# Kernel tuning notes

Measured on AMD Instinct MI355X. Metric: run time of the kernel, lower is better.

Reference implementation:

```python
import jax, jax.numpy as jnp
import numpy as np

IN_FEATURES = 4096
OUT_FEATURES = 8192
LUT_SIZE = 65536  # 256 * 256 two-level codebook


def setup_inputs() -> dict:
    key = jax.random.key(0)
    k_x, k_b, k_f, k_s, k_l = jax.random.split(key, 5)
    x = jax.random.normal(k_x, (2, 256, IN_FEATURES), dtype=jnp.float32)
    base_idx = jax.random.randint(k_b, (OUT_FEATURES, IN_FEATURES), 0, 256, dtype=jnp.int32)
    fine_idx = jax.random.randint(k_f, (OUT_FEATURES, IN_FEATURES), 0, 256, dtype=jnp.int32)
    scale = jax.random.uniform(k_s, (OUT_FEATURES, 1), dtype=jnp.float32)
    lut = jax.random.normal(k_l, (LUT_SIZE,), dtype=jnp.float32)
    return {"x": x, "base_idx": base_idx, "fine_idx": fine_idx, "scale": scale, "lut": lut}


def reference(x, base_idx, fine_idx, scale, lut):
    # Two-level LUT dequant: combined 16-bit index = base*256 + fine
    combined_idx = base_idx * 256 + fine_idx              # [out, in] int32
    weights = lut[combined_idx] * scale                   # [out, in] fp32, per-row scale
    # F.linear(x, weights) == x @ weights.T
    return jnp.einsum('bsi,oi->bso', x, weights)
```

## Files before the change

kernel.cpp:

```cpp
#include <hip/hip_runtime.h>

typedef unsigned short ushort_t;
typedef unsigned int   uint32;
typedef __attribute__((ext_vector_type(8))) short short8;
typedef __attribute__((ext_vector_type(4))) float floatx4;

#define IN_F   4096
#define OUT_F  8192
#define M_TOT  512
#define NB     32
#define BK     64
#define WS     72
#define NITER  (IN_F / BK)

__device__ __forceinline__ ushort_t f2bf(float f) {
    uint32 u = __builtin_bit_cast(uint32, f);
    u += 0x7FFFu + ((u >> 16) & 1u);
    return (ushort_t)(u >> 16);
}

__global__ void cvt_x_kernel(const float* __restrict__ x, ushort_t* __restrict__ xb) {
    int i = (blockIdx.x * 256 + threadIdx.x) * 8;
    float4 v0 = *(const float4*)(x + i);
    float4 v1 = *(const float4*)(x + i + 4);
    short8 s;
    s[0] = (short)f2bf(v0.x); s[1] = (short)f2bf(v0.y);
    s[2] = (short)f2bf(v0.z); s[3] = (short)f2bf(v0.w);
    s[4] = (short)f2bf(v1.x); s[5] = (short)f2bf(v1.y);
    s[6] = (short)f2bf(v1.z); s[7] = (short)f2bf(v1.w);
    *(short8*)(xb + i) = s;
}

template<bool XBF16>
__global__ __launch_bounds__(512)
void ghost_kernel(const float* __restrict__ xf, const ushort_t* __restrict__ xb,
                  const int* __restrict__ base_idx, const int* __restrict__ fine_idx,
                  const float* __restrict__ scale, const float* __restrict__ lut,
                  float* __restrict__ out)
{
    __shared__ ushort_t sh_lut[65536];
    __shared__ ushort_t sh_w[2][NB * WS];

    const int tid = threadIdx.x;
    const int n0  = blockIdx.x * NB;

    for (int i = tid * 4; i < 65536; i += 512 * 4) {
        float4 v = *(const float4*)(lut + i);
        sh_lut[i + 0] = f2bf(v.x);
        sh_lut[i + 1] = f2bf(v.y);
        sh_lut[i + 2] = f2bf(v.z);
        sh_lut[i + 3] = f2bf(v.w);
    }

    const int sn  = tid >> 4;
    const int skq = (tid & 15) * 4;
    const int* bp = base_idx + (size_t)(n0 + sn) * IN_F + skq;
    const int* fp = fine_idx + (size_t)(n0 + sn) * IN_F + skq;

    __syncthreads();

    int4 pb = *(const int4*)(bp);
    int4 pf = *(const int4*)(fp);
    {
        uint32 w0 = (uint32)sh_lut[(pb.x << 8) + pf.x] | ((uint32)sh_lut[(pb.y << 8) + pf.y] << 16);
        uint32 w1 = (uint32)sh_lut[(pb.z << 8) + pf.z] | ((uint32)sh_lut[(pb.w << 8) + pf.w] << 16);
        uint2 wv; wv.x = w0; wv.y = w1;
        *(uint2*)&sh_w[0][sn * WS + skq] = wv;
    }
    pb = *(const int4*)(bp + BK);
    pf = *(const int4*)(fp + BK);
    __syncthreads();

    const int lane = tid & 63;
    const int wave = tid >> 6;
    const int l16  = lane & 15;
    const int quad = lane >> 4;
    const int mrow = wave * 64 + l16;

    floatx4 acc[4][2];
    const floatx4 zero = {0.f, 0.f, 0.f, 0.f};
#pragma unroll
    for (int f = 0; f < 4; ++f) { acc[f][0] = zero; acc[f][1] = zero; }

    const ushort_t* xrow  = XBF16 ? (xb + (size_t)mrow * IN_F + quad * 8) : (const ushort_t*)nullptr;
    const float*    xrowf = XBF16 ? (const float*)nullptr : (xf + (size_t)mrow * IN_F + quad * 8);

    for (int t = 0; t < NITER; ++t) {
        const int k0 = t * BK;

        {
            uint32 w0 = (uint32)sh_lut[(pb.x << 8) + pf.x] | ((uint32)sh_lut[(pb.y << 8) + pf.y] << 16);
            uint32 w1 = (uint32)sh_lut[(pb.z << 8) + pf.z] | ((uint32)sh_lut[(pb.w << 8) + pf.w] << 16);
            uint2 wv; wv.x = w0; wv.y = w1;
            *(uint2*)&sh_w[(t + 1) & 1][sn * WS + skq] = wv;
        }
        {
            const int kk = (t + 2 < NITER ? t + 2 : NITER - 1) * BK;
            pb = *(const int4*)(bp + kk);
            pf = *(const int4*)(fp + kk);
        }

        const ushort_t* wb = sh_w[t & 1];
#pragma unroll
        for (int ks = 0; ks < 2; ++ks) {
            const int kk = k0 + ks * 32;
            short8 b0 = *(const short8*)&wb[l16        * WS + ks * 32 + quad * 8];
            short8 b1 = *(const short8*)&wb[(16 + l16) * WS + ks * 32 + quad * 8];
#pragma unroll
            for (int f = 0; f < 4; ++f) {
                short8 a;
                if (XBF16) {
                    a = *(const short8*)(xrow + (size_t)f * 16 * IN_F + kk);
                } else {
                    const float* p = xrowf + (size_t)f * 16 * IN_F + kk;
                    float4 u0 = *(const float4*)p;
                    float4 u1 = *(const float4*)(p + 4);
                    a[0] = (short)f2bf(u0.x); a[1] = (short)f2bf(u0.y);
                    a[2] = (short)f2bf(u0.z); a[3] = (short)f2bf(u0.w);
                    a[4] = (short)f2bf(u1.x); a[5] = (short)f2bf(u1.y);
                    a[6] = (short)f2bf(u1.z); a[7] = (short)f2bf(u1.w);
                }
                acc[f][0] = __builtin_amdgcn_mfma_f32_16x16x32_bf16(a, b0, acc[f][0], 0, 0, 0);
                acc[f][1] = __builtin_amdgcn_mfma_f32_16x16x32_bf16(a, b1, acc[f][1], 0, 0, 0);
            }
        }
        __syncthreads();
    }

#pragma unroll
    for (int nf = 0; nf < 2; ++nf) {
        const int col = n0 + nf * 16 + l16;
        const float sc = scale[col];
#pragma unroll
        for (int f = 0; f < 4; ++f) {
            const int r0 = wave * 64 + f * 16 + quad * 4;
#pragma unroll
            for (int r = 0; r < 4; ++r) {
                out[(size_t)(r0 + r) * OUT_F + col] = acc[f][nf][r] * sc;
            }
        }
    }
}

extern "C" void kernel_launch(void* const* d_in, const int* in_sizes, int n_in,
                              void* d_out, int out_size, void* d_ws, size_t ws_size,
                              hipStream_t stream) {
    const float* x      = (const float*)d_in[0];
    const int*   bidx   = (const int*)d_in[1];
    const int*   fidx   = (const int*)d_in[2];
    const float* scale  = (const float*)d_in[3];
    const float* lut    = (const float*)d_in[4];
    float*       out    = (float*)d_out;

    const size_t xb_bytes = (size_t)M_TOT * IN_F * sizeof(ushort_t);
    if (ws_size >= xb_bytes) {
        ushort_t* xb = (ushort_t*)d_ws;
        cvt_x_kernel<<<1024, 256, 0, stream>>>(x, xb);
        ghost_kernel<true><<<OUT_F / NB, 512, 0, stream>>>(x, xb, bidx, fidx, scale, lut, out);
    } else {
        ghost_kernel<false><<<OUT_F / NB, 512, 0, stream>>>(x, nullptr, bidx, fidx, scale, lut, out);
    }
}
```

Before: 392.8 us.

## Double block to 1024 threads with 16 waves and BK=128 weight tiles

Raises the thread block from 512 to 1024 threads (16 waves), each wave now covering 32 rows of M instead of 64, and doubles the K tile to 128 so each barrier-separated step does twice the MFMA work. The aim is more latency hiding from extra waves while the 128KB shared LUT still limits the CU to one block, plus fewer syncs per output tile. The trade-off is that each wave reuses its B fragments across fewer A rows, and the double-buffered weight tile uses more shared memory.

```diff
diff --git a/kernel.cpp b/kernel.cpp
--- a/kernel.cpp
+++ b/kernel.cpp
@@ -9,8 +9,8 @@
 #define OUT_F  8192
 #define M_TOT  512
 #define NB     32
-#define BK     64
-#define WS     72
+#define BK     128
+#define WS     136
 #define NITER  (IN_F / BK)
 
 __device__ __forceinline__ ushort_t f2bf(float f) {
@@ -32,7 +32,7 @@
 }
 
 template<bool XBF16>
-__global__ __launch_bounds__(512)
+__global__ __launch_bounds__(1024, 4)
 void ghost_kernel(const float* __restrict__ xf, const ushort_t* __restrict__ xb,
                   const int* __restrict__ base_idx, const int* __restrict__ fine_idx,
                   const float* __restrict__ scale, const float* __restrict__ lut,
@@ -44,7 +44,7 @@
     const int tid = threadIdx.x;
     const int n0  = blockIdx.x * NB;
 
-    for (int i = tid * 4; i < 65536; i += 512 * 4) {
+    for (int i = tid * 4; i < 65536; i += 1024 * 4) {
         float4 v = *(const float4*)(lut + i);
         sh_lut[i + 0] = f2bf(v.x);
         sh_lut[i + 1] = f2bf(v.y);
@@ -52,8 +52,8 @@
         sh_lut[i + 3] = f2bf(v.w);
     }
 
-    const int sn  = tid >> 4;
-    const int skq = (tid & 15) * 4;
+    const int sn  = tid >> 5;
+    const int skq = (tid & 31) * 4;
     const int* bp = base_idx + (size_t)(n0 + sn) * IN_F + skq;
     const int* fp = fine_idx + (size_t)(n0 + sn) * IN_F + skq;
 
@@ -75,13 +75,12 @@
     const int wave = tid >> 6;
     const int l16  = lane & 15;
     const int quad = lane >> 4;
-    const int mrow = wave * 64 + l16;
 
-    floatx4 acc[4][2];
+    floatx4 acc[2][2];
     const floatx4 zero = {0.f, 0.f, 0.f, 0.f};
-#pragma unroll
-    for (int f = 0; f < 4; ++f) { acc[f][0] = zero; acc[f][1] = zero; }
+    acc[0][0] = zero; acc[0][1] = zero; acc[1][0] = zero; acc[1][1] = zero;
 
+    const int mrow = wave * 32 + l16;
     const ushort_t* xrow  = XBF16 ? (xb + (size_t)mrow * IN_F + quad * 8) : (const ushort_t*)nullptr;
     const float*    xrowf = XBF16 ? (const float*)nullptr : (xf + (size_t)mrow * IN_F + quad * 8);
 
@@ -102,27 +101,32 @@
 
         const ushort_t* wb = sh_w[t & 1];
 #pragma unroll
-        for (int ks = 0; ks < 2; ++ks) {
+        for (int ks = 0; ks < 4; ++ks) {
             const int kk = k0 + ks * 32;
             short8 b0 = *(const short8*)&wb[l16        * WS + ks * 32 + quad * 8];
             short8 b1 = *(const short8*)&wb[(16 + l16) * WS + ks * 32 + quad * 8];
-#pragma unroll
-            for (int f = 0; f < 4; ++f) {
-                short8 a;
-                if (XBF16) {
-                    a = *(const short8*)(xrow + (size_t)f * 16 * IN_F + kk);
-                } else {
-                    const float* p = xrowf + (size_t)f * 16 * IN_F + kk;
-                    float4 u0 = *(const float4*)p;
-                    float4 u1 = *(const float4*)(p + 4);
-                    a[0] = (short)f2bf(u0.x); a[1] = (short)f2bf(u0.y);
-                    a[2] = (short)f2bf(u0.z); a[3] = (short)f2bf(u0.w);
-                    a[4] = (short)f2bf(u1.x); a[5] = (short)f2bf(u1.y);
-                    a[6] = (short)f2bf(u1.z); a[7] = (short)f2bf(u1.w);
-                }
-                acc[f][0] = __builtin_amdgcn_mfma_f32_16x16x32_bf16(a, b0, acc[f][0], 0, 0, 0);
-                acc[f][1] = __builtin_amdgcn_mfma_f32_16x16x32_bf16(a, b1, acc[f][1], 0, 0, 0);
+            short8 a0, a1;
+            if (XBF16) {
+                a0 = *(const short8*)(xrow + kk);
+                a1 = *(const short8*)(xrow + (size_t)16 * IN_F + kk);
+            } else {
+                const float* p0 = xrowf + kk;
+                const float* p1 = xrowf + (size_t)16 * IN_F + kk;
+                float4 u0 = *(const float4*)p0, u1 = *(const float4*)(p0 + 4);
+                float4 v0 = *(const float4*)p1, v1 = *(const float4*)(p1 + 4);
+                a0[0] = (short)f2bf(u0.x); a0[1] = (short)f2bf(u0.y);
+                a0[2] = (short)f2bf(u0.z); a0[3] = (short)f2bf(u0.w);
+                a0[4] = (short)f2bf(u1.x); a0[5] = (short)f2bf(u1.y);
+                a0[6] = (short)f2bf(u1.z); a0[7] = (short)f2bf(u1.w);
+                a1[0] = (short)f2bf(v0.x); a1[1] = (short)f2bf(v0.y);
+                a1[2] = (short)f2bf(v0.z); a1[3] = (short)f2bf(v0.w);
+                a1[4] = (short)f2bf(v1.x); a1[5] = (short)f2bf(v1.y);
+                a1[6] = (short)f2bf(v1.z); a1[7] = (short)f2bf(v1.w);
             }
+            acc[0][0] = __builtin_amdgcn_mfma_f32_16x16x32_bf16(a0, b0, acc[0][0], 0, 0, 0);
+            acc[0][1] = __builtin_amdgcn_mfma_f32_16x16x32_bf16(a0, b1, acc[0][1], 0, 0, 0);
+            acc[1][0] = __builtin_amdgcn_mfma_f32_16x16x32_bf16(a1, b0, acc[1][0], 0, 0, 0);
+            acc[1][1] = __builtin_amdgcn_mfma_f32_16x16x32_bf16(a1, b1, acc[1][1], 0, 0, 0);
         }
         __syncthreads();
     }
@@ -132,8 +136,8 @@
         const int col = n0 + nf * 16 + l16;
         const float sc = scale[col];
 #pragma unroll
-        for (int f = 0; f < 4; ++f) {
-            const int r0 = wave * 64 + f * 16 + quad * 4;
+        for (int f = 0; f < 2; ++f) {
+            const int r0 = wave * 32 + f * 16 + quad * 4;
 #pragma unroll
             for (int r = 0; r < 4; ++r) {
                 out[(size_t)(r0 + r) * OUT_F + col] = acc[f][nf][r] * sc;
@@ -156,8 +160,8 @@
     if (ws_size >= xb_bytes) {
         ushort_t* xb = (ushort_t*)d_ws;
         cvt_x_kernel<<<1024, 256, 0, stream>>>(x, xb);
-        ghost_kernel<true><<<OUT_F / NB, 512, 0, stream>>>(x, xb, bidx, fidx, scale, lut, out);
+        ghost_kernel<true><<<OUT_F / NB, 1024, 0, stream>>>(x, xb, bidx, fidx, scale, lut, out);
     } else {
-        ghost_kernel<false><<<OUT_F / NB, 512, 0, stream>>>(x, nullptr, bidx, fidx, scale, lut, out);
+        ghost_kernel<false><<<OUT_F / NB, 1024, 0, stream>>>(x, nullptr, bidx, fidx, scale, lut, out);
     }
 }
```

Result: faster. 383.0 us (-2.5%).
